# Kernel optimization log

Measured on AMD Instinct MI355X. Metric: run time of the kernel, lower is better.

Reference implementation:

```python
import jax, jax.numpy as jnp
import numpy as np

DIM = 1024
HEADS = 16
DH = DIM // HEADS
SEQ = 1024
MEM_LEN = 1024
CMEM_LEN = 256
RATIO = 4
SCALE = DH ** -0.5
LN_EPS = 1e-5


def shift(x):
    # x: [b,h,i,j] -> relative-position shift trick
    b, h, i, j = x.shape
    x = jnp.concatenate([x, jnp.zeros((b, h, i, i), x.dtype)], axis=-1)
    l = i + j - 1
    x = x.reshape(b, h, -1)
    pad = (-x.shape[-1]) % l
    x = jnp.concatenate([x, jnp.zeros((b, h, pad), x.dtype)], axis=-1)
    x = x.reshape(b, h, -1, l)
    return x[:, :, :i, i - 1:]


def layer_norm(x, g, b):
    mu = jnp.mean(x, axis=-1, keepdims=True)
    var = jnp.var(x, axis=-1, keepdims=True)
    return (x - mu) * jax.lax.rsqrt(var + LN_EPS) * g + b


def setup_inputs() -> dict:
    key = jax.random.key(0)
    ks = jax.random.split(key, 12)
    B = 4
    KV = CMEM_LEN + MEM_LEN + SEQ
    std = 0.02
    return {
        'x': jax.random.normal(ks[0], (B, SEQ, DIM), jnp.float32),
        'mem': jax.random.normal(ks[1], (B, MEM_LEN, DIM), jnp.float32),
        'cmem': jax.random.normal(ks[2], (B, CMEM_LEN, DIM), jnp.float32),
        'pos_embed': jax.random.normal(ks[3], (HEADS, KV, DH), jnp.float32),
        'input_mask': jnp.ones((B, SEQ), jnp.bool_),
        'Wq': jax.random.normal(ks[4], (DIM, DIM), jnp.float32) * std,
        'Wkv': jax.random.normal(ks[5], (DIM, 2 * DIM), jnp.float32) * std,
        'Wout': jax.random.normal(ks[6], (DIM, DIM), jnp.float32) * std,
        'bout': jnp.zeros((DIM,), jnp.float32),
        'ln_g': jnp.ones((DIM,), jnp.float32),
        'ln_b': jnp.zeros((DIM,), jnp.float32),
        'conv_w': jax.random.normal(ks[7], (DIM, DIM, RATIO), jnp.float32) * std,
        'conv_b': jnp.zeros((DIM,), jnp.float32),
    }


def reference(x, mem, cmem, pos_embed, input_mask, Wq, Wkv, Wout, bout, ln_g, ln_b, conv_w, conv_b):
    b, t, e = x.shape
    mem_len, cmem_len = mem.shape[1], cmem.shape[1]
    total_mem = mem_len + cmem_len

    q = x @ Wq  # [b,t,e]
    kv_input = jnp.concatenate([cmem, mem, x], axis=1)  # [b,kv,e]
    kv_len = kv_input.shape[1]
    kv = kv_input @ Wkv
    k, v = jnp.split(kv, 2, axis=-1)

    def merge_heads(u):
        return u.reshape(u.shape[0], u.shape[1], HEADS, DH).transpose(0, 2, 1, 3)

    q, k, v = merge_heads(q), merge_heads(k), merge_heads(v)  # [b,h,*,dh]

    dots = jnp.einsum('bhid,bhjd->bhij', q, k) * SCALE  # [b,h,t,kv]
    mask_value = -jnp.finfo(dots.dtype).max

    pe = pos_embed[:, -kv_len:].astype(q.dtype)
    pos_dots = jnp.einsum('bhid,hjd->bhij', q, pe) * SCALE
    dots = dots + shift(pos_dots)

    # input mask (memory columns always visible)
    imask = input_mask[:, None, :, None] & input_mask[:, None, None, :]  # [b,1,t,t]
    imask = jnp.concatenate([jnp.ones((b, 1, t, total_mem), jnp.bool_), imask], axis=-1)
    dots = jnp.where(imask, dots, mask_value)

    # causal mask with memory offset
    causal = jnp.triu(jnp.ones((t, t + total_mem), jnp.bool_), k=1 + total_mem)
    dots = jnp.where(causal[None, None], mask_value, dots)

    attn = jax.nn.softmax(dots, axis=-1)
    out = jnp.einsum('bhij,bhjd->bhid', attn, v)
    out = out.transpose(0, 2, 1, 3).reshape(b, t, -1)
    logits = out @ Wout + bout
    logits = layer_norm(x + logits, ln_g, ln_b)

    # memory update (calc_memory=True, eval mode: no aux reconstruction loss)
    all_mem = jnp.concatenate([mem, x], axis=1)
    old_mem, new_mem = all_mem[:, :-MEM_LEN], all_mem[:, -MEM_LEN:]
    # old_mem length (mem_len+t-MEM_LEN) is a multiple of RATIO here -> no pad needed
    om = old_mem.transpose(0, 2, 1)  # [b,e,L]
    comp = jax.lax.conv_general_dilated(
        om, conv_w, window_strides=(RATIO,), padding='VALID',
        dimension_numbers=('NCH', 'OIH', 'NCH')) + conv_b[None, :, None]
    compressed_mem = comp.transpose(0, 2, 1)  # [b,L/ratio,e]
    all_cmem = jnp.concatenate([cmem, compressed_mem], axis=1)
    new_cmem = all_cmem[:, -CMEM_LEN:]

    aux_loss = jnp.zeros((1,), q.dtype)
    return logits, new_mem, new_cmem, aux_loss
```

## Files before the change

kernel.cpp:

```cpp
#include <hip/hip_runtime.h>
#include <stdint.h>

typedef __attribute__((ext_vector_type(8))) short short8;
typedef __attribute__((ext_vector_type(4))) short short4_;
typedef __attribute__((ext_vector_type(4))) float floatx4;

#define MFMA16(a,b,c) __builtin_amdgcn_mfma_f32_16x16x32_bf16((a),(b),(c),0,0,0)

__device__ __forceinline__ short f2b(float f) {
  union { float f; uint32_t u; } v; v.f = f;
  uint32_t r = v.u + 0x7fffu + ((v.u >> 16) & 1u);
  return (short)(r >> 16);
}

__device__ __forceinline__ unsigned cvt_pk_bf16(float a, float b) {
  unsigned r;
  asm("v_cvt_pk_bf16_f32 %0, %1, %2" : "=v"(r) : "v"(a), "v"(b));
  return r;
}

__device__ __forceinline__ void gload_lds16(const short* g, short* l) {
  __builtin_amdgcn_global_load_lds((const unsigned int*)g, (unsigned int*)l, 16, 0, 0);
}


__global__ __launch_bounds__(256) void pack_kvin(const float* __restrict__ x,
    const float* __restrict__ mem, const float* __restrict__ cmem,
    short* __restrict__ out) {
  long idx = (long)blockIdx.x * 256 + threadIdx.x;
  long base = idx * 4;
  if (base >= 9437184L) return;
  int b = (int)(base / 2359296L);
  int rem = (int)(base - (long)b * 2359296L);
  int r = rem >> 10, c = rem & 1023;
  const float* src;
  if (r < 256)       src = cmem + ((long)b * 256  + r)          * 1024 + c;
  else if (r < 1280) src = mem  + ((long)b * 1024 + (r - 256))  * 1024 + c;
  else               src = x    + ((long)b * 1024 + (r - 1280)) * 1024 + c;
  float4 v = *(const float4*)src;
  short4_ o; o.x = f2b(v.x); o.y = f2b(v.y); o.z = f2b(v.z); o.w = f2b(v.w);
  *(short4_*)(out + base) = o;
}

__global__ __launch_bounds__(256) void pack_cvt(const float* __restrict__ in,
    short* __restrict__ out, long n4) {
  long idx = (long)blockIdx.x * 256 + threadIdx.x;
  if (idx >= n4) return;
  long base = idx * 4;
  float4 v = *(const float4*)(in + base);
  short4_ o; o.x = f2b(v.x); o.y = f2b(v.y); o.z = f2b(v.z); o.w = f2b(v.w);
  *(short4_*)(out + base) = o;
}

__global__ __launch_bounds__(256) void pack_convw(const float* __restrict__ cw,
    short* __restrict__ out) {
  long idx = (long)blockIdx.x * 256 + threadIdx.x;
  long base = idx * 4;
  if (base >= 4194304L) return;
  int co = (int)(base >> 12);
  int r  = (int)(base & 4095);
  int tt = r >> 10, ci = r & 1023;
  const float* s = cw + (long)co * 4096 + tt;
  short4_ o;
  o.x = f2b(s[(ci + 0) * 4]); o.y = f2b(s[(ci + 1) * 4]);
  o.z = f2b(s[(ci + 2) * 4]); o.w = f2b(s[(ci + 3) * 4]);
  *(short4_*)(out + base) = o;
}

__global__ __launch_bounds__(256) void transpose_w(const float* __restrict__ in,
    short* __restrict__ out, int R, int C) {
  __shared__ float tile[32][33];
  int bx = blockIdx.x << 5, by = blockIdx.y << 5;
  int tx = threadIdx.x, ty = threadIdx.y;
#pragma unroll
  for (int yy = 0; yy < 4; ++yy)
    tile[ty + 8 * yy][tx] = in[(long)(by + ty + 8 * yy) * C + bx + tx];
  __syncthreads();
#pragma unroll
  for (int yy = 0; yy < 4; ++yy)
    out[(long)(bx + ty + 8 * yy) * R + by + tx] = f2b(tile[tx][ty + 8 * yy]);
}

__global__ __launch_bounds__(256) void transpose_v(const short* __restrict__ in,
    short* __restrict__ out) {
  __shared__ short tile[32][33];
  int bh = blockIdx.z;
  int j0 = blockIdx.x << 5, d0 = blockIdx.y << 5;
  int tx = threadIdx.x, ty = threadIdx.y;
  const short* ip = in + (long)bh * 147456;
  short* op = out + (long)bh * 147456;
#pragma unroll
  for (int yy = 0; yy < 4; ++yy)
    tile[ty + 8 * yy][tx] = ip[(long)(j0 + ty + 8 * yy) * 64 + d0 + tx];
  __syncthreads();
#pragma unroll
  for (int yy = 0; yy < 4; ++yy)
    op[(long)(d0 + ty + 8 * yy) * 2304 + j0 + tx] = tile[tx][ty + 8 * yy];
}

template<int MODE>
__global__ __launch_bounds__(256) void gemm_bt(
    const short* __restrict__ A, const short* __restrict__ Bt,
    float* __restrict__ Cf, short* __restrict__ Ck, short* __restrict__ Cv,
    const float* __restrict__ bias,
    int M, int N, int K, int a_rpb, long a_bstride, int a_row0, int a_lda) {
  __shared__ __align__(16) short As[128][32];
  __shared__ __align__(16) short Bs[128][32];
  int t = threadIdx.x;
  int w = t >> 6, lane = t & 63;
  int wr = (w >> 1) << 6, wc = (w & 1) << 6;
  int lrow = lane & 15, lk8 = (lane >> 4) << 3, lq4 = (lane >> 4) << 2;
  int rowblk = blockIdx.y << 7, colblk = blockIdx.x << 7;

  floatx4 acc[4][4];
#pragma unroll
  for (int i = 0; i < 4; ++i)
#pragma unroll
    for (int j = 0; j < 4; ++j) acc[i][j] = (floatx4){0.f, 0.f, 0.f, 0.f};

  int srow = (w << 5) + (lane >> 2), kcol = (lane & 3) << 3;
  int gA0 = rowblk + srow, gA1 = gA0 + 16;
  int bA0 = gA0 / a_rpb, rA0 = gA0 - bA0 * a_rpb;
  int bA1 = gA1 / a_rpb, rA1 = gA1 - bA1 * a_rpb;
  const short* a0p = A + bA0 * a_bstride + (long)(a_row0 + rA0) * a_lda + kcol;
  const short* a1p = A + bA1 * a_bstride + (long)(a_row0 + rA1) * a_lda + kcol;
  const short* b0p = Bt + (long)(colblk + srow) * K + kcol;
  const short* b1p = b0p + (long)16 * K;
  short* lA0 = &As[(w << 5)][0];
  short* lA1 = &As[(w << 5) + 16][0];
  short* lB0 = &Bs[(w << 5)][0];
  short* lB1 = &Bs[(w << 5) + 16][0];

  for (int k0 = 0; k0 < K; k0 += 32) {
    __syncthreads();
    gload_lds16(a0p + k0, lA0);
    gload_lds16(a1p + k0, lA1);
    gload_lds16(b0p + k0, lB0);
    gload_lds16(b1p + k0, lB1);
    __syncthreads();
    short8 af[4], bf[4];
#pragma unroll
    for (int mm = 0; mm < 4; ++mm) af[mm] = *(const short8*)(&As[wr + (mm << 4) + lrow][lk8]);
#pragma unroll
    for (int nn = 0; nn < 4; ++nn) bf[nn] = *(const short8*)(&Bs[wc + (nn << 4) + lrow][lk8]);
#pragma unroll
    for (int mm = 0; mm < 4; ++mm)
#pragma unroll
      for (int nn = 0; nn < 4; ++nn)
        acc[mm][nn] = MFMA16(af[mm], bf[nn], acc[mm][nn]);
  }

#pragma unroll
  for (int mm = 0; mm < 4; ++mm) {
#pragma unroll
    for (int nn = 0; nn < 4; ++nn) {
#pragma unroll
      for (int q = 0; q < 4; ++q) {
        int grow = rowblk + wr + (mm << 4) + lq4 + q;
        int gcol = colblk + wc + (nn << 4) + (lane & 15);
        float v = acc[mm][nn][q];
        if (MODE == 0) {
          Cf[(long)grow * N + gcol] = v + bias[gcol];
        } else if (MODE == 1) {
          int b = grow >> 10, i = grow & 1023, hh = gcol >> 6, d = gcol & 63;
          Ck[(((long)(b * 16 + hh)) * 1024 + i) * 64 + d] = f2b(v * 0.125f);
        } else {
          int b = grow / 2304, j = grow - b * 2304;
          if (gcol < 1024) {
            int hh = gcol >> 6, d = gcol & 63;
            Ck[(((long)(b * 16 + hh)) * 2304 + j) * 64 + d] = f2b(v);
          } else {
            int c2 = gcol - 1024, hh = c2 >> 6, d = c2 & 63;
            Cv[(((long)(b * 16 + hh)) * 2304 + j) * 64 + d] = f2b(v);
          }
        }
      }
    }
  }
}

__global__ __launch_bounds__(256) void gemm64_bias(const short* __restrict__ A,
    const short* __restrict__ Bt, float* __restrict__ Cf,
    const float* __restrict__ bias,
    int N, int K, int a_rpb, long a_bstride, int a_lda) {
  __shared__ __align__(16) short As[64][32];
  __shared__ __align__(16) short Bs[64][32];
  int t = threadIdx.x;
  int w = t >> 6, lane = t & 63;
  int wr = (w >> 1) << 5, wc = (w & 1) << 5;
  int lrow = lane & 15, lk8 = (lane >> 4) << 3, lq4 = (lane >> 4) << 2;
  int rowblk = blockIdx.y << 6, colblk = blockIdx.x << 6;
  floatx4 acc[2][2];
#pragma unroll
  for (int i = 0; i < 2; ++i)
#pragma unroll
    for (int j = 0; j < 2; ++j) acc[i][j] = (floatx4){0.f, 0.f, 0.f, 0.f};

  int srow = (w << 4) + (lane >> 2), kcol = (lane & 3) << 3;
  int gA0 = rowblk + srow;
  int bA0 = gA0 / a_rpb, rA0 = gA0 - bA0 * a_rpb;
  const short* a0p = A + bA0 * a_bstride + (long)rA0 * a_lda + kcol;
  const short* b0p = Bt + (long)(colblk + srow) * K + kcol;
  short* lA0 = &As[(w << 4)][0];
  short* lB0 = &Bs[(w << 4)][0];

  for (int k0 = 0; k0 < K; k0 += 32) {
    __syncthreads();
    gload_lds16(a0p + k0, lA0);
    gload_lds16(b0p + k0, lB0);
    __syncthreads();
    short8 af[2], bf[2];
#pragma unroll
    for (int mm = 0; mm < 2; ++mm) af[mm] = *(const short8*)(&As[wr + (mm << 4) + lrow][lk8]);
#pragma unroll
    for (int nn = 0; nn < 2; ++nn) bf[nn] = *(const short8*)(&Bs[wc + (nn << 4) + lrow][lk8]);
#pragma unroll
    for (int mm = 0; mm < 2; ++mm)
#pragma unroll
      for (int nn = 0; nn < 2; ++nn)
        acc[mm][nn] = MFMA16(af[mm], bf[nn], acc[mm][nn]);
  }
#pragma unroll
  for (int mm = 0; mm < 2; ++mm)
#pragma unroll
    for (int nn = 0; nn < 2; ++nn)
#pragma unroll
      for (int q = 0; q < 4; ++q) {
        int grow = rowblk + wr + (mm << 4) + lq4 + q;
        int gcol = colblk + wc + (nn << 4) + (lane & 15);
        Cf[(long)grow * N + gcol] = acc[mm][nn][q] + bias[gcol];
      }
}

__global__ __launch_bounds__(64) void attn_kernel(
    const short* __restrict__ q_r, const short* __restrict__ k_r,
    const short* __restrict__ vt, const short* __restrict__ pe_b,
    short* __restrict__ attn_out) {
  __shared__ float T_skew[16][97];
  __shared__ __align__(16) short P_lds[16][72];
  int p = blockIdx.x;
  int blk = ((p & 7) << 8) | (p >> 3);
  int ib = blk & 31, bh = blk >> 5;
  int b = bh >> 4, h = bh & 15;
  int i0 = ib << 5;
  int lane = threadIdx.x;
  int l = lane & 15, g = lane >> 4;
  int k8 = g << 3;

  const short* qb = q_r + ((long)(bh * 1024 + i0) << 6);
  short8 qf[2][2];
#pragma unroll
  for (int m = 0; m < 2; ++m) {
    qf[m][0] = *(const short8*)(qb + (((m << 4) + l) << 6) + k8);
    qf[m][1] = *(const short8*)(qb + (((m << 4) + l) << 6) + 32 + k8);
  }

  const short* kb = k_r + (long)bh * 147456;
  const short* vb = vt  + (long)bh * 147456;
  const short* pb = pe_b + (long)h * 147456;

  floatx4 o0[4], o1[4];
#pragma unroll
  for (int dc = 0; dc < 4; ++dc) {
    o0[dc] = (floatx4){0.f, 0.f, 0.f, 0.f};
    o1[dc] = (floatx4){0.f, 0.f, 0.f, 0.f};
  }
  float m0r = -1e30f, m1r = -1e30f, l0r = 0.f, l1r = 0.f;

  int ntiles = ((i0 + 1311) >> 6) + 1;

  short8 kfA[4][2], kfB[4][2];
#pragma unroll
  for (int jt = 0; jt < 4; ++jt) {
    const short* kr = kb + ((long)((jt << 4) + l) << 6);
    kfA[jt][0] = *(const short8*)(kr + k8);
    kfA[jt][1] = *(const short8*)(kr + 32 + k8);
  }

  auto chunk = [&](int i0c, short8 (&kf)[4][2], short8 (&vf)[4][2],
                   short8 (&qfm)[2], float& mreg, float& lreg,
                   floatx4 (&oo)[4], int j0) {
    floatx4 s[4];
#pragma unroll
    for (int jt = 0; jt < 4; ++jt) {
      s[jt] = (floatx4){0.f, 0.f, 0.f, 0.f};
      s[jt] = MFMA16(kf[jt][0], qfm[0], s[jt]);
      s[jt] = MFMA16(kf[jt][1], qfm[1], s[jt]);
    }
    int rb = j0 - i0c + 1008;
#pragma unroll
    for (int pt = 0; pt < 5; ++pt) {
      int r = rb + (pt << 4) + l;
      r = r < 2303 ? r : 2303;
      const short* pr = pb + ((long)r << 6);
      floatx4 ta = {0.f, 0.f, 0.f, 0.f};
      ta = MFMA16(qfm[0], *(const short8*)(pr + k8), ta);
      ta = MFMA16(qfm[1], *(const short8*)(pr + 32 + k8), ta);
      int row0 = g << 2;
#pragma unroll
      for (int q = 0; q < 4; ++q)
        T_skew[row0 + q][(pt << 4) + l + row0 + q] = ta[q];
    }
    int lim = i0c + l + 1280 - j0;
    float pv[4][4];
    float mx = -1e30f;
#pragma unroll
    for (int jt = 0; jt < 4; ++jt)
#pragma unroll
      for (int q = 0; q < 4; ++q) {
        int jl = (jt << 4) + (g << 2) + q;
        float v = s[jt][q] + T_skew[l][jl + 15];
        v = (jl > lim) ? -1e30f : v;
        pv[jt][q] = v;
        mx = fmaxf(mx, v);
      }
    mx = fmaxf(mx, __shfl_xor(mx, 16));
    mx = fmaxf(mx, __shfl_xor(mx, 32));
    if (__any(mx - mreg > 8.f)) {
      float nm = fmaxf(mreg, mx);
      float al = __expf(mreg - nm);
#pragma unroll
      for (int dc = 0; dc < 4; ++dc) oo[dc] *= al;
      lreg *= al;
      mreg = nm;
    }
    float rs = 0.f;
#pragma unroll
    for (int jt = 0; jt < 4; ++jt)
#pragma unroll
      for (int q = 0; q < 4; ++q) {
        pv[jt][q] = __expf(pv[jt][q] - mreg);
        rs += pv[jt][q];
      }
    rs += __shfl_xor(rs, 16);
    rs += __shfl_xor(rs, 32);
    lreg += rs;
#pragma unroll
    for (int jt = 0; jt < 4; ++jt) {
      unsigned u0 = cvt_pk_bf16(pv[jt][0], pv[jt][1]);
      unsigned u1 = cvt_pk_bf16(pv[jt][2], pv[jt][3]);
      int c0 = (jt << 4) + (g << 2);
      *(unsigned*)&P_lds[l][c0]     = u0;
      *(unsigned*)&P_lds[l][c0 + 2] = u1;
    }
    short8 pa0 = *(const short8*)&P_lds[l][k8];
    short8 pa1 = *(const short8*)&P_lds[l][32 + k8];
#pragma unroll
    for (int dc = 0; dc < 4; ++dc) {
      oo[dc] = MFMA16(vf[dc][0], pa0, oo[dc]);
      oo[dc] = MFMA16(vf[dc][1], pa1, oo[dc]);
    }
  };

  auto body = [&](short8 (&kfC)[4][2], short8 (&kfN)[4][2], int tt) {
    int j0 = tt << 6;
    short8 vf[4][2];
#pragma unroll
    for (int dc = 0; dc < 4; ++dc) {
      const short* vr = vb + (long)((dc << 4) + l) * 2304 + j0;
      vf[dc][0] = *(const short8*)(vr + k8);
      vf[dc][1] = *(const short8*)(vr + 32 + k8);
    }
    if (tt + 1 < ntiles) {
      int j0n = j0 + 64;
#pragma unroll
      for (int jt = 0; jt < 4; ++jt) {
        const short* kr = kb + ((long)(j0n + (jt << 4) + l) << 6);
        kfN[jt][0] = *(const short8*)(kr + k8);
        kfN[jt][1] = *(const short8*)(kr + 32 + k8);
      }
    }
    if (j0 <= i0 + 1295)
      chunk(i0, kfC, vf, qf[0], m0r, l0r, o0, j0);
    chunk(i0 + 16, kfC, vf, qf[1], m1r, l1r, o1, j0);
  };

  int tt = 0;
  while (true) {
    body(kfA, kfB, tt);
    if (++tt >= ntiles) break;
    body(kfB, kfA, tt);
    if (++tt >= ntiles) break;
  }

#pragma unroll
  for (int m = 0; m < 2; ++m) {
    float invl = 1.f / (m == 0 ? l0r : l1r);
    floatx4* oo = (m == 0) ? o0 : o1;
    long rowbase = ((long)(b * 1024 + i0 + (m << 4) + l) << 10) + (h << 6) + (g << 2);
#pragma unroll
    for (int dc = 0; dc < 4; ++dc) {
      uint2 u;
      u.x = cvt_pk_bf16(oo[dc][0] * invl, oo[dc][1] * invl);
      u.y = cvt_pk_bf16(oo[dc][2] * invl, oo[dc][3] * invl);
      *(uint2*)(attn_out + rowbase + (dc << 4)) = u;
    }
  }
}

__global__ __launch_bounds__(256) void ln_kernel(const float* __restrict__ x,
    const float* __restrict__ lp, const float* __restrict__ g,
    const float* __restrict__ bb, float* __restrict__ out) {
  int row = blockIdx.x, t = threadIdx.x;
  long base = (long)row * 1024 + t * 4;
  float4 a = *(const float4*)(x + base);
  float4 bo = *(const float4*)(lp + base);
  float v0 = a.x + bo.x, v1 = a.y + bo.y, v2 = a.z + bo.z, v3 = a.w + bo.w;
  float s1 = v0 + v1 + v2 + v3;
  float s2 = v0 * v0 + v1 * v1 + v2 * v2 + v3 * v3;
#pragma unroll
  for (int off = 1; off < 64; off <<= 1) {
    s1 += __shfl_xor(s1, off);
    s2 += __shfl_xor(s2, off);
  }
  __shared__ float r1[4], r2[4];
  int w = t >> 6;
  if ((t & 63) == 0) { r1[w] = s1; r2[w] = s2; }
  __syncthreads();
  float S1 = r1[0] + r1[1] + r1[2] + r1[3];
  float S2 = r2[0] + r2[1] + r2[2] + r2[3];
  float mu = S1 * (1.f / 1024.f);
  float var = S2 * (1.f / 1024.f) - mu * mu;
  float rs = rsqrtf(var + 1e-5f);
  float4 gv = *(const float4*)(g + t * 4);
  float4 bv = *(const float4*)(bb + t * 4);
  float4 o;
  o.x = (v0 - mu) * rs * gv.x + bv.x;
  o.y = (v1 - mu) * rs * gv.y + bv.y;
  o.z = (v2 - mu) * rs * gv.z + bv.z;
  o.w = (v3 - mu) * rs * gv.w + bv.w;
  *(float4*)(out + base) = o;
}

__global__ __launch_bounds__(256) void copy_x(const float* __restrict__ x,
    float* __restrict__ outmem, float* __restrict__ aux) {
  long i = (long)blockIdx.x * 256 + threadIdx.x;
  ((float4*)outmem)[i] = ((const float4*)x)[i];
  if (i == 0) aux[0] = 0.f;
}

extern "C" void kernel_launch(void* const* d_in, const int* in_sizes, int n_in,
                              void* d_out, int out_size, void* d_ws, size_t ws_size,
                              hipStream_t stream) {
  const float* x    = (const float*)d_in[0];
  const float* mem  = (const float*)d_in[1];
  const float* cmem = (const float*)d_in[2];
  const float* pe   = (const float*)d_in[3];
  const float* Wq   = (const float*)d_in[5];
  const float* Wkv  = (const float*)d_in[6];
  const float* Wout = (const float*)d_in[7];
  const float* bout = (const float*)d_in[8];
  const float* lng  = (const float*)d_in[9];
  const float* lnb  = (const float*)d_in[10];
  const float* cw   = (const float*)d_in[11];
  const float* cb   = (const float*)d_in[12];

  char* ws = (char*)d_ws;
  short* kvin_b = (short*)(ws + 0);
  short* q_r    = (short*)(ws + 18874368);
  short* k_r    = (short*)(ws + 27262976);
  short* vtp    = (short*)(ws + 46137344);
  short* v_r    = (short*)(ws + 65011712);
  short* pe_b   = (short*)(ws + 83886080);
  short* wq_t   = (short*)(ws + 88604672);
  short* wkv_t  = (short*)(ws + 90701824);
  short* wout_t = (short*)(ws + 94896128);
  short* cw_t   = (short*)(ws + 96993280);
  short* attn_o = (short*)(ws + 105381888);
  float* lpre   = (float*)(ws + 113770496);

  float* out_logits = (float*)d_out;
  float* out_mem    = out_logits + 4194304;
  float* out_cmem   = out_logits + 8388608;
  float* out_aux    = out_logits + 9437184;

  pack_kvin<<<9216, 256, 0, stream>>>(x, mem, cmem, kvin_b);
  pack_cvt<<<2304, 256, 0, stream>>>(pe, pe_b, 589824);
  transpose_w<<<dim3(32, 32), dim3(32, 8), 0, stream>>>(Wq, wq_t, 1024, 1024);
  transpose_w<<<dim3(64, 32), dim3(32, 8), 0, stream>>>(Wkv, wkv_t, 1024, 2048);
  transpose_w<<<dim3(32, 32), dim3(32, 8), 0, stream>>>(Wout, wout_t, 1024, 1024);
  pack_convw<<<4096, 256, 0, stream>>>(cw, cw_t);

  gemm_bt<1><<<dim3(8, 32), 256, 0, stream>>>(kvin_b, wq_t, nullptr, q_r, nullptr,
      nullptr, 4096, 1024, 1024, 1024, 2359296L, 1280, 1024);
  gemm_bt<2><<<dim3(16, 72), 256, 0, stream>>>(kvin_b, wkv_t, nullptr, k_r, v_r,
      nullptr, 9216, 2048, 1024, 2304, 2359296L, 0, 1024);
  transpose_v<<<dim3(72, 2, 64), dim3(32, 8), 0, stream>>>(v_r, vtp);

  attn_kernel<<<2048, 64, 0, stream>>>(q_r, k_r, vtp, pe_b, attn_o);

  gemm_bt<0><<<dim3(8, 32), 256, 0, stream>>>(attn_o, wout_t, lpre, nullptr, nullptr,
      bout, 4096, 1024, 1024, 4096, 0L, 0, 1024);
  ln_kernel<<<4096, 256, 0, stream>>>(x, lpre, lng, lnb, out_logits);

  copy_x<<<4096, 256, 0, stream>>>(x, out_mem, out_aux);

  gemm64_bias<<<dim3(16, 16), 256, 0, stream>>>(kvin_b + 262144, cw_t, out_cmem,
      cb, 1024, 4096, 256, 2359296L, 4096);
}
```

Measured before the change: 657.8 us.

## Split attention KV tiles across four waves per block and split-K the conv GEMM

```diff
diff --git a/kernel.cpp b/kernel.cpp
--- a/kernel.cpp
+++ b/kernel.cpp
@@ -179,9 +179,14 @@
   }
 }
 
-__global__ __launch_bounds__(256) void gemm64_bias(const short* __restrict__ A,
+__global__ __launch_bounds__(256) void init_cmem_bias(const float* __restrict__ cb,
+    float* __restrict__ out) {
+  long base = ((long)blockIdx.x * 256 + threadIdx.x) * 4;
+  *(float4*)(out + base) = *(const float4*)(cb + (base & 1023));
+}
+
+__global__ __launch_bounds__(256) void gemm64_splitk(const short* __restrict__ A,
     const short* __restrict__ Bt, float* __restrict__ Cf,
-    const float* __restrict__ bias,
     int N, int K, int a_rpb, long a_bstride, int a_lda) {
   __shared__ __align__(16) short As[64][32];
   __shared__ __align__(16) short Bs[64][32];
@@ -190,6 +195,7 @@
   int wr = (w >> 1) << 5, wc = (w & 1) << 5;
   int lrow = lane & 15, lk8 = (lane >> 4) << 3, lq4 = (lane >> 4) << 2;
   int rowblk = blockIdx.y << 6, colblk = blockIdx.x << 6;
+  int kbase = blockIdx.z << 10, kend = kbase + 1024;
   floatx4 acc[2][2];
 #pragma unroll
   for (int i = 0; i < 2; ++i)
@@ -204,7 +210,7 @@
   short* lA0 = &As[(w << 4)][0];
   short* lB0 = &Bs[(w << 4)][0];
 
-  for (int k0 = 0; k0 < K; k0 += 32) {
+  for (int k0 = kbase; k0 < kend; k0 += 32) {
     __syncthreads();
     gload_lds16(a0p + k0, lA0);
     gload_lds16(b0p + k0, lB0);
@@ -228,64 +234,71 @@
       for (int q = 0; q < 4; ++q) {
         int grow = rowblk + wr + (mm << 4) + lq4 + q;
         int gcol = colblk + wc + (nn << 4) + (lane & 15);
-        Cf[(long)grow * N + gcol] = acc[mm][nn][q] + bias[gcol];
+        atomicAdd(Cf + (long)grow * N + gcol, acc[mm][nn][q]);
       }
 }
 
-__global__ __launch_bounds__(64) void attn_kernel(
+__global__ __launch_bounds__(256, 4) void attn_kernel(
     const short* __restrict__ q_r, const short* __restrict__ k_r,
     const short* __restrict__ vt, const short* __restrict__ pe_b,
     short* __restrict__ attn_out) {
-  __shared__ float T_skew[16][97];
-  __shared__ __align__(16) short P_lds[16][72];
+  struct WorkT { float T[4][16][97]; short P[4][16][72]; };
+  struct MergeT { float ml[2][32][2]; float O[2][16][66]; };
+  __shared__ union SU { WorkT wk; MergeT mg; } sm;
+
   int p = blockIdx.x;
   int blk = ((p & 7) << 8) | (p >> 3);
   int ib = blk & 31, bh = blk >> 5;
   int b = bh >> 4, h = bh & 15;
   int i0 = ib << 5;
-  int lane = threadIdx.x;
+  int tid = threadIdx.x;
+  int w = tid >> 6, lane = tid & 63;
+  int js = w & 1, rc = w >> 1;
   int l = lane & 15, g = lane >> 4;
   int k8 = g << 3;
-
-  const short* qb = q_r + ((long)(bh * 1024 + i0) << 6);
-  short8 qf[2][2];
-#pragma unroll
-  for (int m = 0; m < 2; ++m) {
-    qf[m][0] = *(const short8*)(qb + (((m << 4) + l) << 6) + k8);
-    qf[m][1] = *(const short8*)(qb + (((m << 4) + l) << 6) + 32 + k8);
-  }
+  int i0c = i0 + (rc << 4);
+
+  float (*Tw)[97] = sm.wk.T[w];
+  short (*Pw)[72] = sm.wk.P[w];
+
+  const short* qb = q_r + ((long)(bh * 1024 + i0c + l) << 6);
+  short8 qf0 = *(const short8*)(qb + k8);
+  short8 qf1 = *(const short8*)(qb + 32 + k8);
 
   const short* kb = k_r + (long)bh * 147456;
   const short* vb = vt  + (long)bh * 147456;
   const short* pb = pe_b + (long)h * 147456;
 
-  floatx4 o0[4], o1[4];
-#pragma unroll
-  for (int dc = 0; dc < 4; ++dc) {
-    o0[dc] = (floatx4){0.f, 0.f, 0.f, 0.f};
-    o1[dc] = (floatx4){0.f, 0.f, 0.f, 0.f};
-  }
-  float m0r = -1e30f, m1r = -1e30f, l0r = 0.f, l1r = 0.f;
+  floatx4 o[4];
+#pragma unroll
+  for (int dc = 0; dc < 4; ++dc) o[dc] = (floatx4){0.f, 0.f, 0.f, 0.f};
+  float m_r = -1e30f, l_r = 0.f;
 
   int ntiles = ((i0 + 1311) >> 6) + 1;
 
-  short8 kfA[4][2], kfB[4][2];
-#pragma unroll
-  for (int jt = 0; jt < 4; ++jt) {
-    const short* kr = kb + ((long)((jt << 4) + l) << 6);
-    kfA[jt][0] = *(const short8*)(kr + k8);
-    kfA[jt][1] = *(const short8*)(kr + 32 + k8);
-  }
-
-  auto chunk = [&](int i0c, short8 (&kf)[4][2], short8 (&vf)[4][2],
-                   short8 (&qfm)[2], float& mreg, float& lreg,
-                   floatx4 (&oo)[4], int j0) {
+  for (int tt = js; tt < ntiles; tt += 2) {
+    int j0 = tt << 6;
+    if (j0 > i0c + 1295) break;
+    short8 kf[4][2];
+#pragma unroll
+    for (int jt = 0; jt < 4; ++jt) {
+      const short* kr = kb + ((long)(j0 + (jt << 4) + l) << 6);
+      kf[jt][0] = *(const short8*)(kr + k8);
+      kf[jt][1] = *(const short8*)(kr + 32 + k8);
+    }
     floatx4 s[4];
 #pragma unroll
     for (int jt = 0; jt < 4; ++jt) {
       s[jt] = (floatx4){0.f, 0.f, 0.f, 0.f};
-      s[jt] = MFMA16(kf[jt][0], qfm[0], s[jt]);
-      s[jt] = MFMA16(kf[jt][1], qfm[1], s[jt]);
+      s[jt] = MFMA16(kf[jt][0], qf0, s[jt]);
+      s[jt] = MFMA16(kf[jt][1], qf1, s[jt]);
+    }
+    short8 vf[4][2];
+#pragma unroll
+    for (int dc = 0; dc < 4; ++dc) {
+      const short* vr = vb + (long)((dc << 4) + l) * 2304 + j0;
+      vf[dc][0] = *(const short8*)(vr + k8);
+      vf[dc][1] = *(const short8*)(vr + 32 + k8);
     }
     int rb = j0 - i0c + 1008;
 #pragma unroll
@@ -294,105 +307,95 @@
       r = r < 2303 ? r : 2303;
       const short* pr = pb + ((long)r << 6);
       floatx4 ta = {0.f, 0.f, 0.f, 0.f};
-      ta = MFMA16(qfm[0], *(const short8*)(pr + k8), ta);
-      ta = MFMA16(qfm[1], *(const short8*)(pr + 32 + k8), ta);
+      ta = MFMA16(qf0, *(const short8*)(pr + k8), ta);
+      ta = MFMA16(qf1, *(const short8*)(pr + 32 + k8), ta);
       int row0 = g << 2;
 #pragma unroll
       for (int q = 0; q < 4; ++q)
-        T_skew[row0 + q][(pt << 4) + l + row0 + q] = ta[q];
+        Tw[row0 + q][(pt << 4) + l + row0 + q] = ta[q];
     }
     int lim = i0c + l + 1280 - j0;
-    float pv[4][4];
     float mx = -1e30f;
 #pragma unroll
     for (int jt = 0; jt < 4; ++jt)
 #pragma unroll
       for (int q = 0; q < 4; ++q) {
         int jl = (jt << 4) + (g << 2) + q;
-        float v = s[jt][q] + T_skew[l][jl + 15];
+        float v = s[jt][q] + Tw[l][jl + 15];
         v = (jl > lim) ? -1e30f : v;
-        pv[jt][q] = v;
+        s[jt][q] = v;
         mx = fmaxf(mx, v);
       }
     mx = fmaxf(mx, __shfl_xor(mx, 16));
     mx = fmaxf(mx, __shfl_xor(mx, 32));
-    if (__any(mx - mreg > 8.f)) {
-      float nm = fmaxf(mreg, mx);
-      float al = __expf(mreg - nm);
-#pragma unroll
-      for (int dc = 0; dc < 4; ++dc) oo[dc] *= al;
-      lreg *= al;
-      mreg = nm;
+    if (__any(mx - m_r > 8.f)) {
+      float nm = fmaxf(m_r, mx);
+      float al = __expf(m_r - nm);
+#pragma unroll
+      for (int dc = 0; dc < 4; ++dc) o[dc] *= al;
+      l_r *= al;
+      m_r = nm;
     }
     float rs = 0.f;
 #pragma unroll
     for (int jt = 0; jt < 4; ++jt)
 #pragma unroll
       for (int q = 0; q < 4; ++q) {
-        pv[jt][q] = __expf(pv[jt][q] - mreg);
-        rs += pv[jt][q];
+        s[jt][q] = __expf(s[jt][q] - m_r);
+        rs += s[jt][q];
       }
     rs += __shfl_xor(rs, 16);
     rs += __shfl_xor(rs, 32);
-    lreg += rs;
+    l_r += rs;
 #pragma unroll
     for (int jt = 0; jt < 4; ++jt) {
-      unsigned u0 = cvt_pk_bf16(pv[jt][0], pv[jt][1]);
-      unsigned u1 = cvt_pk_bf16(pv[jt][2], pv[jt][3]);
+      unsigned u0 = cvt_pk_bf16(s[jt][0], s[jt][1]);
+      unsigned u1 = cvt_pk_bf16(s[jt][2], s[jt][3]);
       int c0 = (jt << 4) + (g << 2);
-      *(unsigned*)&P_lds[l][c0]     = u0;
-      *(unsigned*)&P_lds[l][c0 + 2] = u1;
-    }
-    short8 pa0 = *(const short8*)&P_lds[l][k8];
-    short8 pa1 = *(const short8*)&P_lds[l][32 + k8];
+      *(unsigned*)&Pw[l][c0]     = u0;
+      *(unsigned*)&Pw[l][c0 + 2] = u1;
+    }
+    short8 pa0 = *(const short8*)&Pw[l][k8];
+    short8 pa1 = *(const short8*)&Pw[l][32 + k8];
 #pragma unroll
     for (int dc = 0; dc < 4; ++dc) {
-      oo[dc] = MFMA16(vf[dc][0], pa0, oo[dc]);
-      oo[dc] = MFMA16(vf[dc][1], pa1, oo[dc]);
-    }
-  };
-
-  auto body = [&](short8 (&kfC)[4][2], short8 (&kfN)[4][2], int tt) {
-    int j0 = tt << 6;
-    short8 vf[4][2];
+      o[dc] = MFMA16(vf[dc][0], pa0, o[dc]);
+      o[dc] = MFMA16(vf[dc][1], pa1, o[dc]);
+    }
+  }
+
+  __syncthreads();
+  if (lane < 16) {
+    sm.mg.ml[js][(rc << 4) + l][0] = m_r;
+    sm.mg.ml[js][(rc << 4) + l][1] = l_r;
+  }
+  __syncthreads();
+  float mo = sm.mg.ml[js ^ 1][(rc << 4) + l][0];
+  float lo = sm.mg.ml[js ^ 1][(rc << 4) + l][1];
+  float M  = fmaxf(m_r, mo);
+  float sc = __expf(m_r - M);
+  float L  = l_r * sc + lo * __expf(mo - M);
+  float invL = 1.f / L;
+  if (js == 1) {
+#pragma unroll
+    for (int dc = 0; dc < 4; ++dc)
+#pragma unroll
+      for (int q = 0; q < 4; ++q)
+        sm.mg.O[rc][l][(dc << 4) + (g << 2) + q] = o[dc][q] * sc;
+  }
+  __syncthreads();
+  if (js == 0) {
+    long rowbase = ((long)(b * 1024 + i0c + l) << 10) + (h << 6) + (g << 2);
 #pragma unroll
     for (int dc = 0; dc < 4; ++dc) {
-      const short* vr = vb + (long)((dc << 4) + l) * 2304 + j0;
-      vf[dc][0] = *(const short8*)(vr + k8);
-      vf[dc][1] = *(const short8*)(vr + 32 + k8);
-    }
-    if (tt + 1 < ntiles) {
-      int j0n = j0 + 64;
-#pragma unroll
-      for (int jt = 0; jt < 4; ++jt) {
-        const short* kr = kb + ((long)(j0n + (jt << 4) + l) << 6);
-        kfN[jt][0] = *(const short8*)(kr + k8);
-        kfN[jt][1] = *(const short8*)(kr + 32 + k8);
-      }
-    }
-    if (j0 <= i0 + 1295)
-      chunk(i0, kfC, vf, qf[0], m0r, l0r, o0, j0);
-    chunk(i0 + 16, kfC, vf, qf[1], m1r, l1r, o1, j0);
-  };
-
-  int tt = 0;
-  while (true) {
-    body(kfA, kfB, tt);
-    if (++tt >= ntiles) break;
-    body(kfB, kfA, tt);
-    if (++tt >= ntiles) break;
-  }
-
-#pragma unroll
-  for (int m = 0; m < 2; ++m) {
-    float invl = 1.f / (m == 0 ? l0r : l1r);
-    floatx4* oo = (m == 0) ? o0 : o1;
-    long rowbase = ((long)(b * 1024 + i0 + (m << 4) + l) << 10) + (h << 6) + (g << 2);
-#pragma unroll
-    for (int dc = 0; dc < 4; ++dc) {
+      int c0 = (dc << 4) + (g << 2);
+      float v0 = (o[dc][0] * sc + sm.mg.O[rc][l][c0 + 0]) * invL;
+      float v1 = (o[dc][1] * sc + sm.mg.O[rc][l][c0 + 1]) * invL;
+      float v2 = (o[dc][2] * sc + sm.mg.O[rc][l][c0 + 2]) * invL;
+      float v3 = (o[dc][3] * sc + sm.mg.O[rc][l][c0 + 3]) * invL;
       uint2 u;
-      u.x = cvt_pk_bf16(oo[dc][0] * invl, oo[dc][1] * invl);
-      u.y = cvt_pk_bf16(oo[dc][2] * invl, oo[dc][3] * invl);
+      u.x = cvt_pk_bf16(v0, v1);
+      u.y = cvt_pk_bf16(v2, v3);
       *(uint2*)(attn_out + rowbase + (dc << 4)) = u;
     }
   }
@@ -487,7 +490,7 @@
       nullptr, 9216, 2048, 1024, 2304, 2359296L, 0, 1024);
   transpose_v<<<dim3(72, 2, 64), dim3(32, 8), 0, stream>>>(v_r, vtp);
 
-  attn_kernel<<<2048, 64, 0, stream>>>(q_r, k_r, vtp, pe_b, attn_o);
+  attn_kernel<<<2048, 256, 0, stream>>>(q_r, k_r, vtp, pe_b, attn_o);
 
   gemm_bt<0><<<dim3(8, 32), 256, 0, stream>>>(attn_o, wout_t, lpre, nullptr, nullptr,
       bout, 4096, 1024, 1024, 4096, 0L, 0, 1024);
@@ -495,6 +498,7 @@
 
   copy_x<<<4096, 256, 0, stream>>>(x, out_mem, out_aux);
 
-  gemm64_bias<<<dim3(16, 16), 256, 0, stream>>>(kvin_b + 262144, cw_t, out_cmem,
-      cb, 1024, 4096, 256, 2359296L, 4096);
-}
+  init_cmem_bias<<<1024, 256, 0, stream>>>(cb, out_cmem);
+  gemm64_splitk<<<dim3(16, 16, 4), 256, 0, stream>>>(kvin_b + 262144, cw_t,
+      out_cmem, 1024, 4096, 256, 2359296L, 4096);
+}
```

After: 713.9 us. +8.5%, slower.
